# Optimization experiments

Measured on AMD Instinct MI355X. Metric: run time of the kernel, lower is better.

The kernel has to match this reference:

```python
import jax, jax.numpy as jnp
import numpy as np

B = 8192
I = 1024
H = 1024


def setup_inputs() -> dict:
    key = jax.random.key(0)
    ks = jax.random.split(key, 7)
    s_in = 1.0 / np.sqrt(I)
    s_h = 1.0 / np.sqrt(H)
    return {
        "x_current": jax.random.normal(ks[0], (B, I), dtype=jnp.float32),
        "c_previous": jax.random.normal(ks[1], (B, H), dtype=jnp.float32),
        "h_previous": jax.random.normal(ks[2], (B, H), dtype=jnp.float32),
        # stacked gate weights, order (i, f, o, g); equivalent to 8 small nn.Linear
        "Wx": jax.random.normal(ks[3], (4 * H, I), dtype=jnp.float32) * s_in,
        "bx": jax.random.normal(ks[4], (4 * H,), dtype=jnp.float32) * s_in,
        "Wh": jax.random.normal(ks[5], (4 * H, H), dtype=jnp.float32) * s_h,
        "bh": jax.random.normal(ks[6], (4 * H,), dtype=jnp.float32) * s_h,
    }


def reference(x_current, c_previous, h_previous, Wx, bx, Wh, bh):
    # two fused GEMMs covering all 8 original linears: [B, 4H]
    gates = (jnp.einsum("bi,gi->bg", x_current, Wx) + bx
             + jnp.einsum("bh,gh->bg", h_previous, Wh) + bh)
    i_g, f_g, o_g, g_g = jnp.split(gates, 4, axis=-1)
    input_gate = jax.nn.sigmoid(i_g)
    forget_gate = jax.nn.sigmoid(f_g)
    output_gate = jax.nn.sigmoid(o_g)
    g_current = jnp.tanh(g_g)
    c_current = forget_gate * c_previous + input_gate * g_current
    h_current = output_gate * jnp.tanh(c_current)
    return (c_current, h_current)
```

## Files before the change

### kernel.cpp

```cpp
#include <hip/hip_runtime.h>
#include <hip/hip_bf16.h>

#define Bsz 8192
#define Isz 1024
#define Hsz 1024
#define Ksz 2048
#define Nsz 4096

#define BM 128
#define BN 128
#define BK 32

typedef __attribute__((ext_vector_type(8))) short bf16x8;
typedef __attribute__((ext_vector_type(4))) float f32x4;
typedef __attribute__((ext_vector_type(8))) unsigned short ushort8;

__device__ __forceinline__ void async_copy16(const void* g, void* l) {
  __builtin_amdgcn_global_load_lds(
      (const __attribute__((address_space(1))) void*)g,
      (__attribute__((address_space(3))) void*)l, 16, 0, 0);
}

__device__ __forceinline__ float sigmoid_f(float x) {
  return 1.0f / (1.0f + __expf(-x));
}
__device__ __forceinline__ float tanh_f(float x) {
  x = fminf(15.0f, fmaxf(-15.0f, x));
  const float e = __expf(-2.0f * x);
  return (1.0f - e) / (1.0f + e);
}

__device__ __forceinline__ unsigned short bfc(float f) {
  return __builtin_bit_cast(unsigned short, __float2bfloat16(f));
}
__device__ __forceinline__ ushort8 cvt8v(float4 v0, float4 v1) {
  ushort8 o;
  o[0] = bfc(v0.x); o[1] = bfc(v0.y); o[2] = bfc(v0.z); o[3] = bfc(v0.w);
  o[4] = bfc(v1.x); o[5] = bfc(v1.y); o[6] = bfc(v1.z); o[7] = bfc(v1.w);
  return o;
}

__global__ __launch_bounds__(256) void prep_kernel(
    const float* __restrict__ x, const float* __restrict__ h,
    const float* __restrict__ Wx, const float* __restrict__ Wh,
    const float* __restrict__ bx, const float* __restrict__ bh,
    __hip_bfloat16* __restrict__ Abf, __hip_bfloat16* __restrict__ Wbf,
    float* __restrict__ bsum) {
  const int idx = blockIdx.x * 256 + threadIdx.x;
  const int ATH = (Bsz * Ksz) / 8;
  if (idx < ATH) {
    const int b = idx >> 8;
    const int k = (idx & 255) << 3;
    const float* src = (k < Isz) ? (x + (size_t)b * Isz + k)
                                 : (h + (size_t)b * Hsz + (k - Isz));
    const float4 v0 = ((const float4*)src)[0];
    const float4 v1 = ((const float4*)src)[1];
    *(ushort8*)(Abf + (size_t)b * Ksz + k) = cvt8v(v0, v1);
  } else {
    const int t2 = idx - ATH;
    const int r = t2 >> 8;
    const int k = (t2 & 255) << 3;
    const int hh = r >> 2, g = r & 3;
    const float* src = (k < Isz) ? (Wx + (size_t)(g * Hsz + hh) * Isz + k)
                                 : (Wh + (size_t)(g * Hsz + hh) * Hsz + (k - Isz));
    const float4 v0 = ((const float4*)src)[0];
    const float4 v1 = ((const float4*)src)[1];
    *(ushort8*)(Wbf + (size_t)r * Ksz + k) = cvt8v(v0, v1);
  }
  if (idx < Nsz) {
    const int hh = idx >> 2, g = idx & 3;
    bsum[idx] = bx[g * Hsz + hh] + bh[g * Hsz + hh];
  }
}

__global__ __launch_bounds__(256) void lstm_gemm_kernel(
    const __hip_bfloat16* __restrict__ A,
    const __hip_bfloat16* __restrict__ W,
    const float* __restrict__ bsum,
    const float* __restrict__ c_prev,
    float* __restrict__ c_out,
    float* __restrict__ h_out) {
  __shared__ __hip_bfloat16 As[BM * BK];
  __shared__ __hip_bfloat16 Bs[BN * BK];
  __shared__ float Ew[4][16 * 68];

  const int tid = threadIdx.x;
  const int lane = tid & 63;
  const int wave = tid >> 6;
  const int wm = wave & 1;
  const int wn = wave >> 1;
  const int row0 = blockIdx.x * BM;
  const int col0 = blockIdx.y * BN;

  const __hip_bfloat16* Ag = A + (size_t)row0 * Ksz;
  const __hip_bfloat16* Wg = W + (size_t)col0 * Ksz;

  const int c0 = tid, c1 = tid + 256;
  const int ar0 = c0 >> 2, ak0 = ((c0 & 3) ^ ((c0 >> 3) & 3)) * 8;
  const int ar1 = c1 >> 2, ak1 = ((c1 & 3) ^ ((c1 >> 3) & 3)) * 8;

  f32x4 acc[4][4] = {};

  const int q = lane >> 4;
  const int cl = lane & 15;
  const int jsw = (q ^ ((cl >> 1) & 3)) * 8;

  for (int kt = 0; kt < Ksz; kt += BK) {
    __syncthreads();
    async_copy16(Ag + (size_t)ar0 * Ksz + kt + ak0, (char*)As + c0 * 16);
    async_copy16(Ag + (size_t)ar1 * Ksz + kt + ak1, (char*)As + c1 * 16);
    async_copy16(Wg + (size_t)ar0 * Ksz + kt + ak0, (char*)Bs + c0 * 16);
    async_copy16(Wg + (size_t)ar1 * Ksz + kt + ak1, (char*)Bs + c1 * 16);
    __syncthreads();

    bf16x8 af[4], bfr[4];
#pragma unroll
    for (int i = 0; i < 4; i++)
      af[i] = *(const bf16x8*)(As + (wm * 64 + i * 16 + cl) * BK + jsw);
#pragma unroll
    for (int j = 0; j < 4; j++)
      bfr[j] = *(const bf16x8*)(Bs + (wn * 64 + j * 16 + cl) * BK + jsw);
#pragma unroll
    for (int i = 0; i < 4; i++)
#pragma unroll
      for (int j = 0; j < 4; j++)
        acc[i][j] = __builtin_amdgcn_mfma_f32_16x16x32_bf16(af[i], bfr[j],
                                                            acc[i][j], 0, 0, 0);
  }

  float bj[4];
#pragma unroll
  for (int j = 0; j < 4; j++)
    bj[j] = bsum[col0 + wn * 64 + j * 16 + cl];

  const int hw = (col0 >> 2) + wn * 16;
  const int r16 = lane >> 2;
  const int tt = lane & 3;
  float* E = &Ew[wave][0];

#pragma unroll
  for (int i = 0; i < 4; i++) {
#pragma unroll
    for (int j = 0; j < 4; j++)
#pragma unroll
      for (int r = 0; r < 4; r++)
        E[(q * 4 + r) * 68 + j * 16 + cl] = acc[i][j][r] + bj[j];
    __builtin_amdgcn_wave_barrier();
    const float* Er = E + r16 * 68 + tt * 16;
    const float4 f0 = ((const float4*)Er)[0];
    const float4 f1 = ((const float4*)Er)[1];
    const float4 f2 = ((const float4*)Er)[2];
    const float4 f3 = ((const float4*)Er)[3];

    const int row = row0 + wm * 64 + i * 16 + r16;
    const size_t off = (size_t)row * Hsz + hw + tt * 4;
    const float4 cp4 = *(const float4*)(c_prev + off);
    float4 c4, h4;
    {
      const float cn = sigmoid_f(f0.y) * cp4.x + sigmoid_f(f0.x) * tanh_f(f0.w);
      c4.x = cn; h4.x = sigmoid_f(f0.z) * tanh_f(cn);
    }
    {
      const float cn = sigmoid_f(f1.y) * cp4.y + sigmoid_f(f1.x) * tanh_f(f1.w);
      c4.y = cn; h4.y = sigmoid_f(f1.z) * tanh_f(cn);
    }
    {
      const float cn = sigmoid_f(f2.y) * cp4.z + sigmoid_f(f2.x) * tanh_f(f2.w);
      c4.z = cn; h4.z = sigmoid_f(f2.z) * tanh_f(cn);
    }
    {
      const float cn = sigmoid_f(f3.y) * cp4.w + sigmoid_f(f3.x) * tanh_f(f3.w);
      c4.w = cn; h4.w = sigmoid_f(f3.z) * tanh_f(cn);
    }
    *(float4*)(c_out + off) = c4;
    *(float4*)(h_out + off) = h4;
    __builtin_amdgcn_wave_barrier();
  }
}

extern "C" void kernel_launch(void* const* d_in, const int* in_sizes, int n_in,
                              void* d_out, int out_size, void* d_ws,
                              size_t ws_size, hipStream_t stream) {
  (void)in_sizes; (void)n_in; (void)out_size; (void)ws_size;
  const float* x  = (const float*)d_in[0];
  const float* cp = (const float*)d_in[1];
  const float* hp = (const float*)d_in[2];
  const float* Wx = (const float*)d_in[3];
  const float* bx = (const float*)d_in[4];
  const float* Wh = (const float*)d_in[5];
  const float* bh = (const float*)d_in[6];

  __hip_bfloat16* Abf = (__hip_bfloat16*)d_ws;
  __hip_bfloat16* Wbf = Abf + (size_t)Bsz * Ksz;
  float* bsum = (float*)(Wbf + (size_t)Nsz * Ksz);

  float* c_out = (float*)d_out;
  float* h_out = c_out + (size_t)Bsz * Hsz;

  const int total_threads = (Bsz * Ksz) / 8 + (Nsz * Ksz) / 8;
  prep_kernel<<<total_threads / 256, 256, 0, stream>>>(x, hp, Wx, Wh, bx, bh,
                                                       Abf, Wbf, bsum);
  dim3 grid(Bsz / BM, Nsz / BN);
  lstm_gemm_kernel<<<grid, 256, 0, stream>>>(Abf, Wbf, bsum, cp, c_out, h_out);
}
```

Baseline: 354.9 us.

## Double K-tile depth to 64 and alias epilogue scratch onto GEMM shared memory

Raises the K-step per shared-memory stage from 32 to 64, so each barrier pair and load phase now feeds two MFMA sub-steps. This halves the number of synchronizations per tile. The loader and XOR swizzle are reworked for 8 chunks per row, and the epilogue scratch buffer now reuses the As/Bs storage behind an extra barrier, keeping LDS usage at 32KB. The cost is more data per stage with still no double buffering, which may lengthen load stalls.

```diff
diff --git a/kernel.cpp b/kernel.cpp
--- a/kernel.cpp
+++ b/kernel.cpp
@@ -9,7 +9,7 @@
 
 #define BM 128
 #define BN 128
-#define BK 32
+#define BK 64
 
 typedef __attribute__((ext_vector_type(8))) short bf16x8;
 typedef __attribute__((ext_vector_type(4))) float f32x4;
@@ -80,9 +80,9 @@
     const float* __restrict__ c_prev,
     float* __restrict__ c_out,
     float* __restrict__ h_out) {
-  __shared__ __hip_bfloat16 As[BM * BK];
-  __shared__ __hip_bfloat16 Bs[BN * BK];
-  __shared__ float Ew[4][16 * 68];
+  __shared__ ulong2 smem_raw[2048];
+  __hip_bfloat16* As = (__hip_bfloat16*)smem_raw;
+  __hip_bfloat16* Bs = As + BM * BK;
 
   const int tid = threadIdx.x;
   const int lane = tid & 63;
@@ -95,38 +95,53 @@
   const __hip_bfloat16* Ag = A + (size_t)row0 * Ksz;
   const __hip_bfloat16* Wg = W + (size_t)col0 * Ksz;
 
-  const int c0 = tid, c1 = tid + 256;
-  const int ar0 = c0 >> 2, ak0 = ((c0 & 3) ^ ((c0 >> 3) & 3)) * 8;
-  const int ar1 = c1 >> 2, ak1 = ((c1 & 3) ^ ((c1 >> 3) & 3)) * 8;
+  int srow[4], sofs[4];
+#pragma unroll
+  for (int p = 0; p < 4; p++) {
+    const int c = tid + p * 256;
+    srow[p] = c >> 3;
+    sofs[p] = ((c & 7) ^ ((c >> 3) & 7)) << 3;
+  }
 
   f32x4 acc[4][4] = {};
 
   const int q = lane >> 4;
   const int cl = lane & 15;
-  const int jsw = (q ^ ((cl >> 1) & 3)) * 8;
+  const int phi = cl & 7;
 
   for (int kt = 0; kt < Ksz; kt += BK) {
     __syncthreads();
-    async_copy16(Ag + (size_t)ar0 * Ksz + kt + ak0, (char*)As + c0 * 16);
-    async_copy16(Ag + (size_t)ar1 * Ksz + kt + ak1, (char*)As + c1 * 16);
-    async_copy16(Wg + (size_t)ar0 * Ksz + kt + ak0, (char*)Bs + c0 * 16);
-    async_copy16(Wg + (size_t)ar1 * Ksz + kt + ak1, (char*)Bs + c1 * 16);
+#pragma unroll
+    for (int p = 0; p < 4; p++)
+      async_copy16(Ag + (size_t)srow[p] * Ksz + kt + sofs[p],
+                   (char*)As + (tid + p * 256) * 16);
+#pragma unroll
+    for (int p = 0; p < 4; p++)
+      async_copy16(Wg + (size_t)srow[p] * Ksz + kt + sofs[p],
+                   (char*)Bs + (tid + p * 256) * 16);
     __syncthreads();
 
-    bf16x8 af[4], bfr[4];
-#pragma unroll
-    for (int i = 0; i < 4; i++)
-      af[i] = *(const bf16x8*)(As + (wm * 64 + i * 16 + cl) * BK + jsw);
-#pragma unroll
-    for (int j = 0; j < 4; j++)
-      bfr[j] = *(const bf16x8*)(Bs + (wn * 64 + j * 16 + cl) * BK + jsw);
-#pragma unroll
-    for (int i = 0; i < 4; i++)
+#pragma unroll
+    for (int ks = 0; ks < 2; ks++) {
+      const int jsw = ((ks * 4 + q) ^ phi) << 3;
+      bf16x8 af[4], bfr[4];
+#pragma unroll
+      for (int i = 0; i < 4; i++)
+        af[i] = *(const bf16x8*)(As + (wm * 64 + i * 16 + cl) * BK + jsw);
 #pragma unroll
       for (int j = 0; j < 4; j++)
-        acc[i][j] = __builtin_amdgcn_mfma_f32_16x16x32_bf16(af[i], bfr[j],
-                                                            acc[i][j], 0, 0, 0);
-  }
+        bfr[j] = *(const bf16x8*)(Bs + (wn * 64 + j * 16 + cl) * BK + jsw);
+#pragma unroll
+      for (int i = 0; i < 4; i++)
+#pragma unroll
+        for (int j = 0; j < 4; j++)
+          acc[i][j] = __builtin_amdgcn_mfma_f32_16x16x32_bf16(
+              af[i], bfr[j], acc[i][j], 0, 0, 0);
+    }
+  }
+
+  __syncthreads();
+  float* E = (float*)smem_raw + wave * (16 * 68);
 
   float bj[4];
 #pragma unroll
@@ -136,7 +151,6 @@
   const int hw = (col0 >> 2) + wn * 16;
   const int r16 = lane >> 2;
   const int tt = lane & 3;
-  float* E = &Ew[wave][0];
 
 #pragma unroll
   for (int i = 0; i < 4; i++) {
```

Measured after the change: 334.2 us. 1.06x faster.
